# Kernel tuning notes

Measured on AMD Instinct MI355X. Metric: run time of the kernel, lower is better.

The kernel has to match this reference:

```python
import jax, jax.numpy as jnp
import numpy as np

N, DIM, VOCAB = 16384, 256, 8192  # tokens, complex dim, codebook size


def setup_inputs() -> dict:
    key = jax.random.key(0)
    k1, k2, k3 = jax.random.split(key, 3)
    z_real = jax.random.normal(k1, (N, DIM), dtype=jnp.float32)
    z_imag = jax.random.normal(k2, (N, DIM), dtype=jnp.float32)
    # codebook: [vocab, 2*dim] (orthogonal init in torch; random normal is fine for a numeric reference)
    weight = jax.random.normal(k3, (VOCAB, 2 * DIM), dtype=jnp.float32)
    return {"z_real": z_real, "z_imag": z_imag, "weight": weight}


def reference(z_real, z_imag, weight):
    dim = z_real.shape[-1]
    z_flat = jnp.concatenate([z_real, z_imag], axis=-1)  # [N, 2d]
    # squared euclidean distances (argmin-equivalent to torch.cdist p=2)
    d2 = (jnp.sum(z_flat * z_flat, -1, keepdims=True)
          - 2.0 * (z_flat @ weight.T)
          + jnp.sum(weight * weight, -1)[None, :])  # [N, V]
    indices = jnp.argmin(d2, axis=-1)  # [N]
    z_q = weight[indices]  # [N, 2d]

    commitment_loss = jnp.mean((jax.lax.stop_gradient(z_q) - z_flat) ** 2)
    codebook_loss = jnp.mean((z_q - jax.lax.stop_gradient(z_flat)) ** 2)
    vq_loss = codebook_loss + 0.25 * commitment_loss

    # straight-through estimator
    z_q_st = z_flat + jax.lax.stop_gradient(z_q - z_flat)

    # perplexity from code usage histogram (== mean of one-hot encodings)
    vocab = weight.shape[0]
    counts = jnp.zeros((vocab,), jnp.float32).at[indices].add(1.0)
    avg_probs = counts / z_flat.shape[0]
    perplexity = jnp.exp(-jnp.sum(avg_probs * jnp.log(avg_probs + 1e-10)))

    z_q_c = jax.lax.complex(z_q_st[..., :dim], z_q_st[..., dim:])
    return (z_q_c, vq_loss, perplexity)
```

## Files before the change

### kernel.cpp

```cpp
#include <hip/hip_runtime.h>

#define N_TOK   16384
#define CDIM    256
#define KDIM    512
#define VOCAB   8192

#define SLICES  8
#define SL_V    (VOCAB / SLICES)
#define BMM     64
#define BNN     128
#define BKK     64

typedef __attribute__((ext_vector_type(8))) short short8v;
typedef __attribute__((ext_vector_type(4))) float f32x4;

typedef const __attribute__((address_space(1))) unsigned int* gp_t;
typedef __attribute__((address_space(3))) unsigned int* lp_t;
__device__ __forceinline__ void gl16(const void* g, void* l) {
    __builtin_amdgcn_global_load_lds((gp_t)g, (lp_t)l, 16, 0, 0);
}

__device__ __forceinline__ unsigned int bf2(float a, float b) {
    unsigned int ua = __float_as_uint(a); ua = (ua + 0x7FFF + ((ua >> 16) & 1)) >> 16;
    unsigned int ub = __float_as_uint(b); ub = (ub + 0x7FFF + ((ub >> 16) & 1)) >> 16;
    return (ub << 16) | ua;
}

__global__ __launch_bounds__(256) void vq_zconv(const float* __restrict__ zr,
                                                const float* __restrict__ zi,
                                                unsigned short* __restrict__ zc) {
    int t = blockIdx.x * 256 + threadIdx.x;
    int e = t * 8;
    int tok = e >> 9, c = e & 511;
    const float* src = (c < CDIM) ? (zr + (size_t)tok * CDIM + c)
                                  : (zi + (size_t)tok * CDIM + (c - CDIM));
    float4 x = ((const float4*)src)[0];
    float4 y = ((const float4*)src)[1];
    uint4 o = make_uint4(bf2(x.x, x.y), bf2(x.z, x.w), bf2(y.x, y.y), bf2(y.z, y.w));
    *(uint4*)(zc + e) = o;
}

__global__ __launch_bounds__(256) void vq_wconv(const float* __restrict__ w,
                                                unsigned short* __restrict__ wb,
                                                float* __restrict__ wnorm,
                                                float* __restrict__ counts,
                                                float* __restrict__ lossAcc) {
    int gid = blockIdx.x * 256 + threadIdx.x;
    int row = gid >> 6, l = gid & 63;
    const float* src = w + (size_t)row * KDIM + l * 8;
    float4 x = ((const float4*)src)[0];
    float4 y = ((const float4*)src)[1];
    float s = x.x*x.x + x.y*x.y + x.z*x.z + x.w*x.w
            + y.x*y.x + y.y*y.y + y.z*y.z + y.w*y.w;
    uint4 o = make_uint4(bf2(x.x, x.y), bf2(x.z, x.w), bf2(y.x, y.y), bf2(y.z, y.w));
    *(uint4*)(wb + (size_t)row * KDIM + l * 8) = o;
    #pragma unroll
    for (int off = 32; off > 0; off >>= 1) s += __shfl_down(s, off);
    if (l == 0) { wnorm[row] = s; counts[row] = 0.f; }
    if (gid == 0) *lossAcc = 0.f;
}

__global__ __launch_bounds__(256) void vq_argmin_mfma(const unsigned short* __restrict__ zc,
                                                      const unsigned short* __restrict__ wb,
                                                      const float* __restrict__ wnorm,
                                                      float* __restrict__ sbV,
                                                      int* __restrict__ sbI) {
    __shared__ unsigned short Asm[2][BMM * BKK];
    __shared__ unsigned short Bsm[2][BNN * BKK];
    __shared__ float sV[2][BMM];
    __shared__ int   sI[2][BMM];
    __shared__ float runV[BMM];
    __shared__ int   runI[BMM];

    const int tid = threadIdx.x;
    const int l   = tid & 63, wv = tid >> 6;
    const int wm  = wv >> 1,  wn = wv & 1;
    const int slice = blockIdx.x & (SLICES - 1);
    const int tok0  = (blockIdx.x >> 3) * BMM;
    const int code0 = slice * SL_V;

    if (tid < BMM) { runV[tid] = 3.4e38f; runI[tid] = 0; }

    const int l15 = l & 15, lhi = l >> 4;

    for (int v0 = 0; v0 < SL_V; v0 += BNN) {
        f32x4 acc[2][4] = {};

        auto STAGE = [&](int buf, int k0) {
            #pragma unroll
            for (int i = 0; i < 2; ++i) {
                int e = i * 2048 + tid * 8;
                int r = e >> 6, c = e & 63;
                gl16(zc + (size_t)(tok0 + r) * KDIM + k0 + c,
                     (void*)&Asm[buf][i * 2048 + wv * 512]);
            }
            #pragma unroll
            for (int i = 0; i < 4; ++i) {
                int e = i * 2048 + tid * 8;
                int r = e >> 6, c = e & 63;
                gl16(wb + (size_t)(code0 + v0 + r) * KDIM + k0 + c,
                     (void*)&Bsm[buf][i * 2048 + wv * 512]);
            }
        };

        STAGE(0, 0);
        __syncthreads();
        for (int ks = 0; ks < KDIM / BKK; ++ks) {
            int cur = ks & 1;
            if (ks < KDIM / BKK - 1) STAGE(cur ^ 1, (ks + 1) * BKK);
            #pragma unroll
            for (int c = 0; c < 2; ++c) {
                short8v a[2], b[4];
                #pragma unroll
                for (int m = 0; m < 2; ++m)
                    a[m] = *(const short8v*)&Asm[cur][(wm * 32 + m * 16 + l15) * 64 + c * 32 + lhi * 8];
                #pragma unroll
                for (int n = 0; n < 4; ++n)
                    b[n] = *(const short8v*)&Bsm[cur][(wn * 64 + n * 16 + l15) * 64 + c * 32 + lhi * 8];
                #pragma unroll
                for (int m = 0; m < 2; ++m)
                    #pragma unroll
                    for (int n = 0; n < 4; ++n)
                        acc[m][n] = __builtin_amdgcn_mfma_f32_16x16x32_bf16(a[m], b[n], acc[m][n], 0, 0, 0);
            }
            __syncthreads();
        }

        const int ccolbase = code0 + v0 + wn * 64 + l15;
        float wn4[4];
        #pragma unroll
        for (int n = 0; n < 4; ++n) wn4[n] = wnorm[ccolbase + n * 16];

        #pragma unroll
        for (int m = 0; m < 2; ++m) {
            #pragma unroll
            for (int r = 0; r < 4; ++r) {
                float best = 3.4e38f; int bi = 0x7fffffff;
                #pragma unroll
                for (int n = 0; n < 4; ++n) {
                    float d = wn4[n] - 2.f * acc[m][n][r];
                    int ci = ccolbase + n * 16;
                    if (d < best) { best = d; bi = ci; }
                }
                #pragma unroll
                for (int mk = 1; mk < 16; mk <<= 1) {
                    float ov = __shfl_xor(best, mk);
                    int   oi = __shfl_xor(bi, mk);
                    if (ov < best || (ov == best && oi < bi)) { best = ov; bi = oi; }
                }
                if (l15 == 0) {
                    int row = wm * 32 + m * 16 + lhi * 4 + r;
                    sV[wn][row] = best; sI[wn][row] = bi;
                }
            }
        }
        __syncthreads();
        if (tid < BMM) {
            float va = sV[0][tid]; int ia = sI[0][tid];
            float vb = sV[1][tid]; int ib = sI[1][tid];
            if (vb < va || (vb == va && ib < ia)) { va = vb; ia = ib; }
            if (va < runV[tid] || (va == runV[tid] && ia < runI[tid])) { runV[tid] = va; runI[tid] = ia; }
        }
    }

    if (tid < BMM) {
        sbV[slice * N_TOK + tok0 + tid] = runV[tid];
        sbI[slice * N_TOK + tok0 + tid] = runI[tid];
    }
}

__global__ __launch_bounds__(256) void vq_reduce(const float* __restrict__ sbV,
                                                 const int* __restrict__ sbI,
                                                 int* __restrict__ idx,
                                                 float* __restrict__ counts) {
    int t = blockIdx.x * 256 + threadIdx.x;
    float bv = sbV[t]; int bi = sbI[t];
    #pragma unroll
    for (int s = 1; s < SLICES; ++s) {
        float v = sbV[s * N_TOK + t];
        int   i = sbI[s * N_TOK + t];
        if (v < bv || (v == bv && i < bi)) { bv = v; bi = i; }
    }
    idx[t] = bi;
    atomicAdd(&counts[bi], 1.0f);
}

__global__ __launch_bounds__(256) void vq_gather(const float* __restrict__ zr,
                                                 const float* __restrict__ zi,
                                                 const float* __restrict__ w,
                                                 const int* __restrict__ idx,
                                                 float* __restrict__ out,
                                                 float* __restrict__ lossAcc,
                                                 int nTokOut) {
    const int lane = threadIdx.x & 63;
    const int wv = threadIdx.x >> 6;
    const int tokBase = blockIdx.x * 16 + wv * 4;
    float s = 0.f;
    for (int t = 0; t < 4; ++t) {
        int tok = tokBase + t;
        int bi = idx[tok];
        const float4* wre = (const float4*)(w + (size_t)bi * KDIM);
        const float4* wim = (const float4*)(w + (size_t)bi * KDIM + CDIM);
        const float4* ar4 = (const float4*)(zr + (size_t)tok * CDIM);
        const float4* ai4 = (const float4*)(zi + (size_t)tok * CDIM);
        float4 qr = wre[lane], qi = wim[lane], ar = ar4[lane], ai = ai4[lane];
        float d;
        d = qr.x - ar.x; s += d * d;  d = qr.y - ar.y; s += d * d;
        d = qr.z - ar.z; s += d * d;  d = qr.w - ar.w; s += d * d;
        d = qi.x - ai.x; s += d * d;  d = qi.y - ai.y; s += d * d;
        d = qi.z - ai.z; s += d * d;  d = qi.w - ai.w; s += d * d;
        if (tok < nTokOut) {
            float4 o0 = make_float4(qr.x, qi.x, qr.y, qi.y);
            float4 o1 = make_float4(qr.z, qi.z, qr.w, qi.w);
            float4* ob = (float4*)(out + (size_t)tok * 2 * CDIM);
            ob[lane * 2]     = o0;
            ob[lane * 2 + 1] = o1;
        }
    }
    #pragma unroll
    for (int off = 32; off > 0; off >>= 1) s += __shfl_down(s, off);
    __shared__ float ls[4];
    if (lane == 0) ls[wv] = s;
    __syncthreads();
    if (threadIdx.x == 0) atomicAdd(lossAcc, ls[0] + ls[1] + ls[2] + ls[3]);
}

__global__ __launch_bounds__(256) void vq_final(const float* __restrict__ counts,
                                                const float* __restrict__ lossAcc,
                                                float* __restrict__ scal) {
    __shared__ float red[256];
    float s = 0.f;
    for (int i = threadIdx.x; i < VOCAB; i += 256) {
        float p = counts[i] * (1.0f / 16384.0f);
        s += p * logf(p + 1e-10f);
    }
    red[threadIdx.x] = s;
    __syncthreads();
    for (int off = 128; off > 0; off >>= 1) {
        if (threadIdx.x < off) red[threadIdx.x] += red[threadIdx.x + off];
        __syncthreads();
    }
    if (threadIdx.x == 0) {
        scal[0] = lossAcc[0] * (1.25f / 8388608.0f);
        scal[1] = expf(-red[0]);
    }
}

extern "C" void kernel_launch(void* const* d_in, const int* in_sizes, int n_in,
                              void* d_out, int out_size, void* d_ws, size_t ws_size,
                              hipStream_t stream) {
    const float* zr = (const float*)d_in[0];
    const float* zi = (const float*)d_in[1];
    const float* w  = (const float*)d_in[2];
    float* out = (float*)d_out;
    float* fws = (float*)d_ws;

    float* wnorm   = fws;
    float* counts  = fws + 8192;
    float* lossAcc = fws + 16384;
    int*   idx     = (int*)(fws + 16400);
    float* sbV     = fws + 32784;
    int*   sbI     = (int*)(fws + 163856);
    unsigned short* zc = (unsigned short*)(fws + 294928);
    unsigned short* wb = (unsigned short*)(fws + 294928 + 4194304);

    int nTokOut = (out_size - 2) / (2 * CDIM);
    if (nTokOut > N_TOK) nTokOut = N_TOK;

    vq_zconv<<<4096, 256, 0, stream>>>(zr, zi, zc);
    vq_wconv<<<2048, 256, 0, stream>>>(w, wb, wnorm, counts, lossAcc);
    vq_argmin_mfma<<<(N_TOK / BMM) * SLICES, 256, 0, stream>>>(zc, wb, wnorm, sbV, sbI);
    vq_reduce<<<N_TOK / 256, 256, 0, stream>>>(sbV, sbI, idx, counts);
    vq_gather<<<N_TOK / 16, 256, 0, stream>>>(zr, zi, w, idx, out, lossAcc, nTokOut);
    vq_final<<<1, 256, 0, stream>>>(counts, lossAcc, out + (out_size - 2));
}
```

Baseline: 475.0 us.

## Enlarge argmin GEMM tiles to 256x256 with swizzled LDS and cross-tile prefetch

New measurement: 391.3 us. -17.6%, faster.

```diff
diff --git a/kernel.cpp b/kernel.cpp
--- a/kernel.cpp
+++ b/kernel.cpp
@@ -5,11 +5,12 @@
 #define KDIM    512
 #define VOCAB   8192
 
-#define SLICES  8
+#define SLICES  4
 #define SL_V    (VOCAB / SLICES)
-#define BMM     64
-#define BNN     128
-#define BKK     64
+#define BM      256
+#define BN      256
+#define BK      64
+#define NKT     (KDIM / BK)
 
 typedef __attribute__((ext_vector_type(8))) short short8v;
 typedef __attribute__((ext_vector_type(4))) float f32x4;
@@ -60,87 +61,135 @@
     if (gid == 0) *lossAcc = 0.f;
 }
 
-__global__ __launch_bounds__(256) void vq_argmin_mfma(const unsigned short* __restrict__ zc,
-                                                      const unsigned short* __restrict__ wb,
-                                                      const float* __restrict__ wnorm,
-                                                      float* __restrict__ sbV,
-                                                      int* __restrict__ sbI) {
-    __shared__ unsigned short Asm[2][BMM * BKK];
-    __shared__ unsigned short Bsm[2][BNN * BKK];
-    __shared__ float sV[2][BMM];
-    __shared__ int   sI[2][BMM];
-    __shared__ float runV[BMM];
-    __shared__ int   runI[BMM];
+__global__ __launch_bounds__(512, 2) void vq_argmin_mfma(const unsigned short* __restrict__ zc,
+                                                         const unsigned short* __restrict__ wb,
+                                                         const float* __restrict__ wnorm,
+                                                         float* __restrict__ sbV,
+                                                         int* __restrict__ sbI) {
+    __shared__ unsigned short Ab[2][2][8192];
+    __shared__ unsigned short Bb[2][2][8192];
+    __shared__ float sV[4][BM];
+    __shared__ int   sI[4][BM];
+    __shared__ float runV[BM];
+    __shared__ int   runI[BM];
 
     const int tid = threadIdx.x;
-    const int l   = tid & 63, wv = tid >> 6;
-    const int wm  = wv >> 1,  wn = wv & 1;
+    const int l   = tid & 63, w = tid >> 6;
+    const int wm  = w >> 2,  wn = w & 3;
     const int slice = blockIdx.x & (SLICES - 1);
-    const int tok0  = (blockIdx.x >> 3) * BMM;
+    const int tok0  = (blockIdx.x >> 2) * BM;
     const int code0 = slice * SL_V;
-
-    if (tid < BMM) { runV[tid] = 3.4e38f; runI[tid] = 0; }
-
     const int l15 = l & 15, lhi = l >> 4;
-
-    for (int v0 = 0; v0 < SL_V; v0 += BNN) {
-        f32x4 acc[2][4] = {};
-
-        auto STAGE = [&](int buf, int k0) {
+    const int bh = wn >> 1, brow0 = (wn & 1) * 64;
+    const int rstage = tid >> 3, sstage = tid & 7;
+
+    for (int i = tid; i < BM; i += 512) { runV[i] = 3.4e38f; runI[i] = 0; }
+
+    auto STAGE = [&](int buf, int k0, int v0) {
+        #pragma unroll
+        for (int h = 0; h < 2; ++h)
             #pragma unroll
             for (int i = 0; i < 2; ++i) {
-                int e = i * 2048 + tid * 8;
-                int r = e >> 6, c = e & 63;
-                gl16(zc + (size_t)(tok0 + r) * KDIM + k0 + c,
-                     (void*)&Asm[buf][i * 2048 + wv * 512]);
+                int r = i * 64 + rstage;
+                int cs = (sstage ^ (r & 7)) * 8;
+                gl16(zc + (size_t)(tok0 + h * 128 + r) * KDIM + k0 + cs,
+                     (void*)&Ab[buf][h][i * 4096 + (w << 9)]);
             }
-            #pragma unroll
-            for (int i = 0; i < 4; ++i) {
-                int e = i * 2048 + tid * 8;
-                int r = e >> 6, c = e & 63;
-                gl16(wb + (size_t)(code0 + v0 + r) * KDIM + k0 + c,
-                     (void*)&Bsm[buf][i * 2048 + wv * 512]);
+        #pragma unroll
+        for (int h = 0; h < 2; ++h)
+            #pragma unroll
+            for (int i = 0; i < 2; ++i) {
+                int r = i * 64 + rstage;
+                int cs = (sstage ^ (r & 7)) * 8;
+                gl16(wb + (size_t)(code0 + v0 + h * 128 + r) * KDIM + k0 + cs,
+                     (void*)&Bb[buf][h][i * 4096 + (w << 9)]);
             }
-        };
-
-        STAGE(0, 0);
-        __syncthreads();
-        for (int ks = 0; ks < KDIM / BKK; ++ks) {
-            int cur = ks & 1;
-            if (ks < KDIM / BKK - 1) STAGE(cur ^ 1, (ks + 1) * BKK);
-            #pragma unroll
-            for (int c = 0; c < 2; ++c) {
-                short8v a[2], b[4];
-                #pragma unroll
-                for (int m = 0; m < 2; ++m)
-                    a[m] = *(const short8v*)&Asm[cur][(wm * 32 + m * 16 + l15) * 64 + c * 32 + lhi * 8];
-                #pragma unroll
-                for (int n = 0; n < 4; ++n)
-                    b[n] = *(const short8v*)&Bsm[cur][(wn * 64 + n * 16 + l15) * 64 + c * 32 + lhi * 8];
-                #pragma unroll
-                for (int m = 0; m < 2; ++m)
+    };
+    auto LDA = [&](int buf, int m, int c) -> short8v {
+        int row = m * 16 + l15;
+        return *(const short8v*)&Ab[buf][wm][row * 64 + (((c * 4 + lhi) ^ (row & 7)) * 8)];
+    };
+    auto LDB = [&](int buf, int n, int c) -> short8v {
+        int row = brow0 + n * 16 + l15;
+        return *(const short8v*)&Bb[buf][bh][row * 64 + (((c * 4 + lhi) ^ (row & 7)) * 8)];
+    };
+
+    for (int v0 = 0; v0 < SL_V; v0 += BN) {
+        f32x4 acc[8][4] = {};
+        if (v0 == 0) { STAGE(0, 0, 0); __syncthreads(); }
+
+        int buf = 0;
+        #pragma unroll 1
+        for (int kt = 0; kt < NKT; ++kt) {
+            if (kt < NKT - 1)        STAGE(buf ^ 1, (kt + 1) * BK, v0);
+            else if (v0 + BN < SL_V) STAGE(buf ^ 1, 0, v0 + BN);
+
+            short8v a[4][2], b[2][2];
+            #pragma unroll
+            for (int m = 0; m < 4; ++m) { a[m][0] = LDA(buf, m, 0); a[m][1] = LDA(buf, m, 1); }
+            #pragma unroll
+            for (int n = 0; n < 2; ++n) { b[n][0] = LDB(buf, n, 0); b[n][1] = LDB(buf, n, 1); }
+            __builtin_amdgcn_s_setprio(1);
+            #pragma unroll
+            for (int m = 0; m < 4; ++m)
+                #pragma unroll
+                for (int n = 0; n < 2; ++n)
                     #pragma unroll
-                    for (int n = 0; n < 4; ++n)
-                        acc[m][n] = __builtin_amdgcn_mfma_f32_16x16x32_bf16(a[m], b[n], acc[m][n], 0, 0, 0);
-            }
+                    for (int c = 0; c < 2; ++c)
+                        acc[m][n] = __builtin_amdgcn_mfma_f32_16x16x32_bf16(a[m][c], b[n][c], acc[m][n], 0, 0, 0);
+            __builtin_amdgcn_s_setprio(0);
+            #pragma unroll
+            for (int n = 0; n < 2; ++n) { b[n][0] = LDB(buf, n + 2, 0); b[n][1] = LDB(buf, n + 2, 1); }
+            __builtin_amdgcn_s_setprio(1);
+            #pragma unroll
+            for (int m = 0; m < 4; ++m)
+                #pragma unroll
+                for (int n = 0; n < 2; ++n)
+                    #pragma unroll
+                    for (int c = 0; c < 2; ++c)
+                        acc[m][n + 2] = __builtin_amdgcn_mfma_f32_16x16x32_bf16(a[m][c], b[n][c], acc[m][n + 2], 0, 0, 0);
+            __builtin_amdgcn_s_setprio(0);
+            #pragma unroll
+            for (int m = 0; m < 4; ++m) { a[m][0] = LDA(buf, m + 4, 0); a[m][1] = LDA(buf, m + 4, 1); }
+            __builtin_amdgcn_s_setprio(1);
+            #pragma unroll
+            for (int m = 0; m < 4; ++m)
+                #pragma unroll
+                for (int n = 0; n < 2; ++n)
+                    #pragma unroll
+                    for (int c = 0; c < 2; ++c)
+                        acc[m + 4][n + 2] = __builtin_amdgcn_mfma_f32_16x16x32_bf16(a[m][c], b[n][c], acc[m + 4][n + 2], 0, 0, 0);
+            __builtin_amdgcn_s_setprio(0);
+            #pragma unroll
+            for (int n = 0; n < 2; ++n) { b[n][0] = LDB(buf, n, 0); b[n][1] = LDB(buf, n, 1); }
+            __builtin_amdgcn_s_setprio(1);
+            #pragma unroll
+            for (int m = 0; m < 4; ++m)
+                #pragma unroll
+                for (int n = 0; n < 2; ++n)
+                    #pragma unroll
+                    for (int c = 0; c < 2; ++c)
+                        acc[m + 4][n] = __builtin_amdgcn_mfma_f32_16x16x32_bf16(a[m][c], b[n][c], acc[m + 4][n], 0, 0, 0);
+            __builtin_amdgcn_s_setprio(0);
+
             __syncthreads();
+            buf ^= 1;
         }
 
-        const int ccolbase = code0 + v0 + wn * 64 + l15;
+        const int cb = code0 + v0 + wn * 64 + l15;
         float wn4[4];
         #pragma unroll
-        for (int n = 0; n < 4; ++n) wn4[n] = wnorm[ccolbase + n * 16];
+        for (int n = 0; n < 4; ++n) wn4[n] = wnorm[cb + n * 16];
 
         #pragma unroll
-        for (int m = 0; m < 2; ++m) {
-            #pragma unroll
-            for (int r = 0; r < 4; ++r) {
+        for (int m = 0; m < 8; ++m) {
+            #pragma unroll
+            for (int j = 0; j < 4; ++j) {
                 float best = 3.4e38f; int bi = 0x7fffffff;
                 #pragma unroll
                 for (int n = 0; n < 4; ++n) {
-                    float d = wn4[n] - 2.f * acc[m][n][r];
-                    int ci = ccolbase + n * 16;
-                    if (d < best) { best = d; bi = ci; }
+                    float d = wn4[n] - 2.f * acc[m][n][j];
+                    if (d < best) { best = d; bi = cb + n * 16; }
                 }
                 #pragma unroll
                 for (int mk = 1; mk < 16; mk <<= 1) {
@@ -149,21 +198,25 @@
                     if (ov < best || (ov == best && oi < bi)) { best = ov; bi = oi; }
                 }
                 if (l15 == 0) {
-                    int row = wm * 32 + m * 16 + lhi * 4 + r;
+                    int row = wm * 128 + m * 16 + lhi * 4 + j;
                     sV[wn][row] = best; sI[wn][row] = bi;
                 }
             }
         }
         __syncthreads();
-        if (tid < BMM) {
-            float va = sV[0][tid]; int ia = sI[0][tid];
-            float vb = sV[1][tid]; int ib = sI[1][tid];
-            if (vb < va || (vb == va && ib < ia)) { va = vb; ia = ib; }
-            if (va < runV[tid] || (va == runV[tid] && ia < runI[tid])) { runV[tid] = va; runI[tid] = ia; }
+        if (tid < BM) {
+            float bv = sV[0][tid]; int bi = sI[0][tid];
+            #pragma unroll
+            for (int s = 1; s < 4; ++s) {
+                float v = sV[s][tid]; int i2 = sI[s][tid];
+                if (v < bv || (v == bv && i2 < bi)) { bv = v; bi = i2; }
+            }
+            if (bv < runV[tid] || (bv == runV[tid] && bi < runI[tid])) { runV[tid] = bv; runI[tid] = bi; }
         }
-    }
-
-    if (tid < BMM) {
+        __syncthreads();
+    }
+
+    if (tid < BM) {
         sbV[slice * N_TOK + tok0 + tid] = runV[tid];
         sbI[slice * N_TOK + tok0 + tid] = runI[tid];
     }
@@ -269,7 +322,7 @@
 
     vq_zconv<<<4096, 256, 0, stream>>>(zr, zi, zc);
     vq_wconv<<<2048, 256, 0, stream>>>(w, wb, wnorm, counts, lossAcc);
-    vq_argmin_mfma<<<(N_TOK / BMM) * SLICES, 256, 0, stream>>>(zc, wb, wnorm, sbV, sbI);
+    vq_argmin_mfma<<<(N_TOK / BM) * SLICES, 512, 0, stream>>>(zc, wb, wnorm, sbV, sbI);
     vq_reduce<<<N_TOK / 256, 256, 0, stream>>>(sbV, sbI, idx, counts);
     vq_gather<<<N_TOK / 16, 256, 0, stream>>>(zr, zi, w, idx, out, lossAcc, nTokOut);
     vq_final<<<1, 256, 0, stream>>>(counts, lossAcc, out + (out_size - 2));
```
